# Kernel tuning notes

Measured on AMD Instinct MI355X. Metric: run time of the kernel, lower is better.

Reference implementation:

```python
import jax, jax.numpy as jnp
import numpy as np

N, B, D, K, H = 30000, 16, 32, 8, 8
DIST = 5.0
EPS = 1e-6


def setup_inputs() -> dict:
    key = jax.random.key(0)
    ks = jax.random.split(key, 16)
    sc = 1.0 / np.sqrt(D)
    inp = {
        'pos': jax.random.uniform(ks[0], (N, 3), jnp.float32) * 20.0,
        'node_features': jax.random.normal(ks[1], (N, D), jnp.float32),
        'batch': jnp.sort(jax.random.randint(ks[2], (N,), 0, B, dtype=jnp.int32)),
        'bessel_weights': jnp.linspace(jnp.pi, K * jnp.pi, K).astype(jnp.float32),
        'init_dummy': jax.random.normal(ks[3], (D,), jnp.float32),
        'Wq_dummy': jax.random.normal(ks[4], (D, D), jnp.float32) * sc,
        'Wq_graph': jax.random.normal(ks[5], (D, D), jnp.float32) * sc,
        'Wdot': jax.random.normal(ks[6], (D, D), jnp.float32) * sc,
        'W1_kd': jax.random.normal(ks[7], (K, H), jnp.float32) / np.sqrt(K),
        'W2_kd': jax.random.normal(ks[8], (H, D * D), jnp.float32) / np.sqrt(H),
        'W1_vd': jax.random.normal(ks[9], (K, H), jnp.float32) / np.sqrt(K),
        'W2_vd': jax.random.normal(ks[10], (H, D * D), jnp.float32) / np.sqrt(H),
        'W1_kg': jax.random.normal(ks[11], (K, H), jnp.float32) / np.sqrt(K),
        'W2_kg': jax.random.normal(ks[12], (H, D * D), jnp.float32) / np.sqrt(H),
        'W1_vg': jax.random.normal(ks[13], (K, H), jnp.float32) / np.sqrt(K),
        'W2_vg': jax.random.normal(ks[14], (H, D * D), jnp.float32) / np.sqrt(H),
    }
    return inp


def reference(pos, node_features, batch, bessel_weights, init_dummy,
              Wq_dummy, Wq_graph, Wdot,
              W1_kd, W2_kd, W1_vd, W2_vd, W1_kg, W2_kg, W1_vg, W2_vg):
    scale = 1.0 / np.sqrt(D)

    # --- dummy edge features: per-batch z extents + bessel basis ---
    z = pos[:, 2]                                            # [N]
    z_min = jax.ops.segment_min(z, batch, num_segments=B)    # [B]
    z_max = jax.ops.segment_max(z, batch, num_segments=B)    # [B]
    bot_len = z - z_min[batch] + DIST                        # [N]
    top_len = z_max[batch] + DIST - z                        # [N]

    def bessel(x):  # [N] -> [N,K]
        return jnp.sin(bessel_weights * x[:, None]) / (x[:, None] + EPS)

    edge = jnp.stack([bessel(bot_len), bessel(top_len)], axis=1)  # [N,2,K]

    # --- init dummy node features [B, 2, D] ---
    dummy = jnp.broadcast_to(init_dummy, (B, 2, D))

    def gen_w(W1, W2):  # conditional weight generator (silu MLP)
        return (jax.nn.silu(edge @ W1) @ W2).reshape(N, 2, D, D)

    # --- dummy nodes attend over graph nodes (segment softmax) ---
    wk = gen_w(W1_kd, W2_kd)                                 # [N,2,D,D]
    wv = gen_w(W1_vd, W2_vd)
    q = (dummy @ Wq_dummy)[batch]                            # [N,2,D]
    k = jnp.einsum('nd,nsde->nse', node_features, wk)        # [N,2,D]
    v = jnp.einsum('nd,nsde->nse', node_features, wv)
    s = jnp.einsum('nsq,qk,nsk->ns', q, Wdot, k) * scale     # [N,2]
    m = jax.ops.segment_max(s, batch, num_segments=B)
    e = jnp.exp(s - m[batch])
    zsum = jax.ops.segment_sum(e, batch, num_segments=B)
    attn = e / zsum[batch]                                   # [N,2]
    dummy_new = dummy + jax.ops.segment_sum(attn[..., None] * v, batch, num_segments=B)

    # --- graph nodes attend over (2) dummy nodes ---
    wkg = gen_w(W1_kg, W2_kg)
    wvg = gen_w(W1_vg, W2_vg)
    d_per = dummy_new[batch]                                 # [N,2,D]
    kg = jnp.einsum('nsd,nsde->nse', d_per, wkg)
    vg = jnp.einsum('nsd,nsde->nse', d_per, wvg)
    qg = node_features @ Wq_graph                            # [N,D]
    sg = jnp.einsum('nq,qk,nsk->ns', qg, Wdot, kg) * scale   # [N,2]
    ag = jax.nn.softmax(sg, axis=1)
    x_new = node_features + jnp.einsum('ns,nsd->nd', ag, vg)  # [N,D]
    return x_new
```

## Files before the change

### kernel.cpp

```cpp
#include <hip/hip_runtime.h>
#include <math.h>

#define NN 30000
#define DIST_C 5.0f
#define EPS_C 1e-6f
#define SCALE_C 0.17677669529663687f

#define WS_ZMIN 0
#define WS_ZMAX 16
#define WS_ZSUM 32
#define WS_T    64
#define WS_PK   8256
#define WS_WC   8512
#define WS_AKG  9536
#define WS_AVG  17728

#define NPT 32

__device__ __forceinline__ float silu(float x) { return x / (1.0f + __expf(-x)); }

__device__ __forceinline__ void bessel_edges(float bw0, float x0, float x1, float edge[2][8]) {
    float xs[2]; xs[0] = x0; xs[1] = x1;
#pragma unroll
    for (int s = 0; s < 2; ++s) {
        float x = xs[s];
        float inv = 1.0f / (x + EPS_C);
        float th = bw0 * x;
        float sk, ck;
        __sincosf(th, &sk, &ck);
        float c2 = 2.0f * ck;
        float skm1 = 0.0f;
#pragma unroll
        for (int k = 0; k < 8; ++k) {
            edge[s][k] = sk * inv;
            float nx = c2 * sk - skm1;
            skm1 = sk; sk = nx;
        }
    }
}

__global__ __launch_bounds__(256) void k_pre(const float* __restrict__ pos,
                                             const int* __restrict__ batch,
                                             const float* __restrict__ init_dummy,
                                             const float* __restrict__ Wq_dummy,
                                             const float* __restrict__ Wdot,
                                             const float* __restrict__ W2_kd,
                                             const float* __restrict__ Wq_graph,
                                             float* __restrict__ ws) {
    int t = threadIdx.x, blk = blockIdx.x;
    if (blk < 16) {
        __shared__ int bnd2[2];
        __shared__ float r[8];
        if (t < 2) {
            int target = blk + t;
            int lo = 0, hi = NN;
            while (lo < hi) { int mid = (lo + hi) >> 1; if (batch[mid] < target) lo = mid + 1; else hi = mid; }
            bnd2[t] = lo;
        }
        __syncthreads();
        int s0 = bnd2[0], s1 = bnd2[1];
        float zmn = 3.4e38f, zmx = -3.4e38f;
        for (int i = s0 + t; i < s1; i += 256) {
            float v = pos[3 * i + 2];
            zmn = fminf(zmn, v); zmx = fmaxf(zmx, v);
        }
#pragma unroll
        for (int off = 1; off < 64; off <<= 1) {
            zmn = fminf(zmn, __shfl_xor(zmn, off, 64));
            zmx = fmaxf(zmx, __shfl_xor(zmx, off, 64));
        }
        if ((t & 63) == 0) { r[(t >> 6) * 2] = zmn; r[(t >> 6) * 2 + 1] = zmx; }
        __syncthreads();
        if (t == 0) {
            ws[WS_ZMIN + blk] = fminf(fminf(r[0], r[2]), fminf(r[4], r[6]));
            ws[WS_ZMAX + blk] = fmaxf(fmaxf(r[1], r[3]), fmaxf(r[5], r[7]));
        }
    } else if (blk == 16) {
        __shared__ float qv[32], qW[32];
        if (t < 32) {
            float acc = 0.f;
            for (int d = 0; d < 32; ++d) acc += init_dummy[d] * Wq_dummy[d * 32 + t];
            qv[t] = acc;
        }
        __syncthreads();
        if (t < 32) {
            float acc = 0.f;
            for (int e = 0; e < 32; ++e) acc += qv[e] * Wdot[e * 32 + t];
            qW[t] = acc;
        }
        __syncthreads();
        int h = t >> 5, d = t & 31;
        float acc = 0.f;
        for (int e = 0; e < 32; ++e) acc += W2_kd[h * 1024 + d * 32 + e] * qW[e];
        ws[WS_PK + t] = acc;
    } else if (blk == 17) {
        for (int i = t; i < 1024; i += 256) {
            int d = i >> 5, e = i & 31;
            float acc = 0.f;
            for (int m = 0; m < 32; ++m) acc += Wq_graph[d * 32 + m] * Wdot[m * 32 + e];
            ws[WS_WC + i] = acc;
        }
    } else {
        int idx = blk - 18;
        ws[WS_T + idx * 512 + t] = 0.f;
        ws[WS_T + idx * 512 + 256 + t] = 0.f;
        if (idx == 0 && t < 32) ws[WS_ZSUM + t] = 0.f;
    }
}

__global__ __launch_bounds__(256) void k_phase1(const float* __restrict__ pos,
                                                const int* __restrict__ batch,
                                                const float* __restrict__ nf,
                                                const float* __restrict__ bw,
                                                const float* __restrict__ W1_kd,
                                                const float* __restrict__ W1_vd,
                                                float* __restrict__ ws) {
    __shared__ __align__(16) float Fl[NPT * 36];
    __shared__ float Lw[NPT * 17];
    __shared__ int   Lb[NPT];
    __shared__ __align__(16) float Pk[256];
    __shared__ float W1kd[64], W1vd[64], zsl[32];
    int t = threadIdx.x;
    if (t < 64) { W1kd[t] = W1_kd[t]; W1vd[t] = W1_vd[t]; }
    Pk[t] = ws[WS_PK + t];
    if (t < 32) zsl[t] = 0.f;

    int li = t >> 3, g = t & 7;
    int n0 = blockIdx.x * NPT;
    int n = n0 + li;
    bool valid = n < NN;
    float4 fv4 = make_float4(0.f, 0.f, 0.f, 0.f);
    int b = 0;
    if (valid) {
        b = batch[n];
        fv4 = ((const float4*)nf)[n * 8 + g];
        ((float4*)(Fl + li * 36))[g] = fv4;
        if (g == 0) Lb[li] = b;
    } else {
        if (g == 0) Lb[li] = -1;
    }
    __syncthreads();

    if (valid) {
        float z = pos[3 * n + 2];
        float zminb = ws[WS_ZMIN + b];
        float zmaxb = ws[WS_ZMAX + b];
        float edge[2][8];
        bessel_edges(bw[0], z - zminb + DIST_C, zmaxb + DIST_C - z, edge);

        float up[8];
        const float4* Pk4 = (const float4*)Pk;
#pragma unroll
        for (int h = 0; h < 8; ++h) {
            float4 p = Pk4[h * 8 + g];
            up[h] = fv4.x * p.x + fv4.y * p.y + fv4.z * p.z + fv4.w * p.w;
        }
        float kd0, kd1;
        {
            float p0 = 0.f, p1 = 0.f;
#pragma unroll
            for (int k = 0; k < 8; ++k) {
                float w = W1kd[k * 8 + g];
                p0 += edge[0][k] * w;
                p1 += edge[1][k] * w;
            }
            kd0 = silu(p0); kd1 = silu(p1);
        }
        int lanebase = (t & 63) & 56;
        float sp0 = 0.f, sp1 = 0.f;
#pragma unroll
        for (int h = 0; h < 8; ++h) {
            sp0 += __shfl(kd0, lanebase + h, 64) * up[h];
            sp1 += __shfl(kd1, lanebase + h, 64) * up[h];
        }
#pragma unroll
        for (int m = 1; m < 8; m <<= 1) {
            sp0 += __shfl_xor(sp0, m, 64);
            sp1 += __shfl_xor(sp1, m, 64);
        }
        float ev0 = __expf(sp0 * SCALE_C);
        float ev1 = __expf(sp1 * SCALE_C);
        if (g == 0) {
            atomicAdd(&zsl[b * 2 + 0], ev0);
            atomicAdd(&zsl[b * 2 + 1], ev1);
        }
        float q0 = 0.f, q1 = 0.f;
#pragma unroll
        for (int k = 0; k < 8; ++k) {
            float w = W1vd[k * 8 + g];
            q0 += edge[0][k] * w;
            q1 += edge[1][k] * w;
        }
        Lw[li * 17 + g]     = ev0 * silu(q0);
        Lw[li * 17 + 8 + g] = ev1 * silu(q1);
    }
    __syncthreads();
    if (t < 32 && zsl[t] != 0.f) atomicAdd(&ws[WS_ZSUM + t], zsl[t]);

    int count = NN - n0; if (count > NPT) count = NPT;
    int bf = Lb[0], bl = Lb[count - 1];
    int sh = t & 15, dp = t >> 4;
    for (int b2 = bf; b2 <= bl; ++b2) {
        float a0 = 0.f, a1 = 0.f;
        for (int i = 0; i < count; ++i) {
            if (Lb[i] != b2) continue;
            float w = Lw[i * 17 + sh];
            float2 x = *(const float2*)(Fl + i * 36 + 2 * dp);
            a0 += w * x.x;
            a1 += w * x.y;
        }
        float* Tb = ws + WS_T + b2 * 512 + sh * 32 + 2 * dp;
        atomicAdd(&Tb[0], a0);
        atomicAdd(&Tb[1], a1);
    }
}

__global__ __launch_bounds__(256) void k_batch(const float* __restrict__ init_dummy,
                                               const float* __restrict__ W2_vd,
                                               const float* __restrict__ W2_kg,
                                               const float* __restrict__ W2_vg,
                                               float* __restrict__ ws) {
    int bs = blockIdx.x;
    int b = bs >> 1, s = bs & 1;
    int t = threadIdx.x;
    __shared__ float Tl[256];
    __shared__ float part[256];
    __shared__ float dn[32];
    Tl[t] = ws[WS_T + b * 512 + s * 256 + t];
    __syncthreads();
    {
        int h = t >> 5, e = t & 31;
        float acc = 0.f;
#pragma unroll
        for (int d = 0; d < 32; ++d) acc += Tl[h * 32 + d] * W2_vd[h * 1024 + d * 32 + e];
        part[t] = acc;
    }
    __syncthreads();
    if (t < 32) {
        float acc = 0.f;
#pragma unroll
        for (int h = 0; h < 8; ++h) acc += part[h * 32 + t];
        float zs = ws[WS_ZSUM + b * 2 + s];
        dn[t] = init_dummy[t] + acc / zs;
    }
    __syncthreads();
    {
        int h = t >> 5, e = t & 31;
        float ak = 0.f, av = 0.f;
#pragma unroll
        for (int d = 0; d < 32; ++d) {
            float dv = dn[d];
            ak += dv * W2_kg[h * 1024 + d * 32 + e];
            av += dv * W2_vg[h * 1024 + d * 32 + e];
        }
        ws[WS_AKG + b * 512 + s * 256 + t] = ak;
        ws[WS_AVG + b * 512 + s * 256 + t] = av;
    }
}

__global__ __launch_bounds__(256) void k_fin(const float* __restrict__ pos,
                                             const int* __restrict__ batch,
                                             const float* __restrict__ nf,
                                             const float* __restrict__ bw,
                                             const float* __restrict__ W1_kg,
                                             const float* __restrict__ W1_vg,
                                             const float* __restrict__ ws,
                                             float* __restrict__ out) {
    __shared__ __align__(16) float Wc[1024];
    __shared__ __align__(16) float Fl[NPT * 36];
    __shared__ int   Lb[NPT];
    __shared__ float W1kg[64], W1vg[64];
    __shared__ __align__(16) float AK[2][512], AV[2][512];

    int t = threadIdx.x;
    int li = t >> 3, g = t & 7;
    int lanebase = (t & 63) & 56;
    {
        const float4* Wg4 = (const float4*)(ws + WS_WC);
        ((float4*)Wc)[t] = Wg4[t];
    }
    if (t < 64) { W1kg[t] = W1_kg[t]; W1vg[t] = W1_vg[t]; }

    int n0 = blockIdx.x * NPT;
    int n = n0 + li;
    int count = NN - n0; if (count > NPT) count = NPT;
    bool valid = li < count;
    float4 fv4 = make_float4(0.f, 0.f, 0.f, 0.f);
    float z = 0.f;
    int b = 0;
    if (valid) {
        b = batch[n];
        fv4 = ((const float4*)nf)[n * 8 + g];
        ((float4*)(Fl + li * 36))[g] = fv4;
        z = pos[3 * n + 2];
        if (g == 0) Lb[li] = b;
    }
    __syncthreads();
    int bf = Lb[0], bl = Lb[count - 1];
    int nseg = (bl != bf) ? 2 : 1;

    for (int sl = 0; sl < nseg; ++sl) {
        int bb = sl ? bl : bf;
        const float4* Ag = (const float4*)(ws + WS_AKG + bb * 512);
        const float4* Vg = (const float4*)(ws + WS_AVG + bb * 512);
        if (t < 128) ((float4*)AK[sl])[t] = Ag[t];
        else         ((float4*)AV[sl])[t - 128] = Vg[t - 128];
    }
    __syncthreads();

    if (!valid) return;
    int slot = (b == bf) ? 0 : 1;
    const float4* Ak4 = (const float4*)AK[slot];
    const float4* Av4 = (const float4*)AV[slot];
    const float4* Wc4 = (const float4*)Wc;

    float zminb = ws[WS_ZMIN + b];
    float zmaxb = ws[WS_ZMAX + b];
    float edge[2][8];
    bessel_edges(bw[0], z - zminb + DIST_C, zmaxb + DIST_C - z, edge);

    float sk0, sk1, sv0, sv1;
    {
        float pk0 = 0.f, pk1 = 0.f, pv0 = 0.f, pv1 = 0.f;
#pragma unroll
        for (int k = 0; k < 8; ++k) {
            float wk = W1kg[k * 8 + g];
            float wv = W1vg[k * 8 + g];
            pk0 += edge[0][k] * wk; pk1 += edge[1][k] * wk;
            pv0 += edge[0][k] * wv; pv1 += edge[1][k] * wv;
        }
        sk0 = silu(pk0); sk1 = silu(pk1);
        sv0 = silu(pv0); sv1 = silu(pv1);
    }
    float4 q4 = make_float4(0.f, 0.f, 0.f, 0.f);
    const float* myF = Fl + li * 36;
#pragma unroll
    for (int d = 0; d < 32; ++d) {
        float fd = myF[d];
        float4 w = Wc4[d * 8 + g];
        q4.x += fd * w.x; q4.y += fd * w.y; q4.z += fd * w.z; q4.w += fd * w.w;
    }
    float p0 = 0.f, p1 = 0.f;
#pragma unroll
    for (int h = 0; h < 8; ++h) {
        float4 a0 = Ak4[h * 8 + g];
        float4 a1 = Ak4[64 + h * 8 + g];
        float d0 = q4.x * a0.x + q4.y * a0.y + q4.z * a0.z + q4.w * a0.w;
        float d1 = q4.x * a1.x + q4.y * a1.y + q4.z * a1.z + q4.w * a1.w;
        p0 += __shfl(sk0, lanebase + h, 64) * d0;
        p1 += __shfl(sk1, lanebase + h, 64) * d1;
    }
#pragma unroll
    for (int m = 1; m < 8; m <<= 1) {
        p0 += __shfl_xor(p0, m, 64);
        p1 += __shfl_xor(p1, m, 64);
    }
    float sg0 = p0 * SCALE_C, sg1 = p1 * SCALE_C;
    float mx = fmaxf(sg0, sg1);
    float e0 = __expf(sg0 - mx), e1 = __expf(sg1 - mx);
    float inv = 1.0f / (e0 + e1);
    float ag0 = e0 * inv, ag1 = e1 * inv;

    float4 x4 = fv4;
#pragma unroll
    for (int h = 0; h < 8; ++h) {
        float w0 = ag0 * __shfl(sv0, lanebase + h, 64);
        float w1 = ag1 * __shfl(sv1, lanebase + h, 64);
        float4 a0 = Av4[h * 8 + g];
        float4 a1 = Av4[64 + h * 8 + g];
        x4.x += w0 * a0.x + w1 * a1.x;
        x4.y += w0 * a0.y + w1 * a1.y;
        x4.z += w0 * a0.z + w1 * a1.z;
        x4.w += w0 * a0.w + w1 * a1.w;
    }
    ((float4*)out)[n * 8 + g] = x4;
}

extern "C" void kernel_launch(void* const* d_in, const int* in_sizes, int n_in,
                              void* d_out, int out_size, void* d_ws, size_t ws_size,
                              hipStream_t stream) {
    const float* pos        = (const float*)d_in[0];
    const float* nf         = (const float*)d_in[1];
    const int*   batch      = (const int*)d_in[2];
    const float* bw         = (const float*)d_in[3];
    const float* init_dummy = (const float*)d_in[4];
    const float* Wq_dummy   = (const float*)d_in[5];
    const float* Wq_graph   = (const float*)d_in[6];
    const float* Wdot       = (const float*)d_in[7];
    const float* W1_kd      = (const float*)d_in[8];
    const float* W2_kd      = (const float*)d_in[9];
    const float* W1_vd      = (const float*)d_in[10];
    const float* W2_vd      = (const float*)d_in[11];
    const float* W1_kg      = (const float*)d_in[12];
    const float* W2_kg      = (const float*)d_in[13];
    const float* W1_vg      = (const float*)d_in[14];
    const float* W2_vg      = (const float*)d_in[15];
    float* ws  = (float*)d_ws;
    float* out = (float*)d_out;

    int nblk = (NN + NPT - 1) / NPT;
    hipLaunchKernelGGL(k_pre, dim3(34), dim3(256), 0, stream,
                       pos, batch, init_dummy, Wq_dummy, Wdot, W2_kd, Wq_graph, ws);
    hipLaunchKernelGGL(k_phase1, dim3(nblk), dim3(256), 0, stream,
                       pos, batch, nf, bw, W1_kd, W1_vd, ws);
    hipLaunchKernelGGL(k_batch, dim3(32), dim3(256), 0, stream,
                       init_dummy, W2_vd, W2_kg, W2_vg, ws);
    hipLaunchKernelGGL(k_fin, dim3(nblk), dim3(256), 0, stream,
                       pos, batch, nf, bw, W1_kg, W1_vg, ws, out);
}
```

Baseline: 120.5 us.

## Split dummy-side work across threads: 16 lanes per node, 512-thread blocks

Both per-node kernels now give each node 16 threads instead of 8. Each thread handles one dummy side and one hidden unit, with float2 feature slices, so the two-side Bessel and SiLU work is split across lanes rather than done twice per thread. The phase-1 segmented reduction is rewritten: __syncthreads_count finds the batch boundary and replaces the Lb scan and per-batch loop with at most two linear passes. This aims at more parallelism and less per-thread register and serial work. The cost is a wider shuffle reduction and 512-thread blocks, and the reduction assumes each block spans at most two batch segments.

```diff
diff --git a/kernel.cpp b/kernel.cpp
--- a/kernel.cpp
+++ b/kernel.cpp
@@ -19,23 +19,18 @@
 
 __device__ __forceinline__ float silu(float x) { return x / (1.0f + __expf(-x)); }
 
-__device__ __forceinline__ void bessel_edges(float bw0, float x0, float x1, float edge[2][8]) {
-    float xs[2]; xs[0] = x0; xs[1] = x1;
-#pragma unroll
-    for (int s = 0; s < 2; ++s) {
-        float x = xs[s];
-        float inv = 1.0f / (x + EPS_C);
-        float th = bw0 * x;
-        float sk, ck;
-        __sincosf(th, &sk, &ck);
-        float c2 = 2.0f * ck;
-        float skm1 = 0.0f;
-#pragma unroll
-        for (int k = 0; k < 8; ++k) {
-            edge[s][k] = sk * inv;
-            float nx = c2 * sk - skm1;
-            skm1 = sk; sk = nx;
-        }
+__device__ __forceinline__ void bessel_edge1(float bw0, float x, float edge[8]) {
+    float inv = 1.0f / (x + EPS_C);
+    float th = bw0 * x;
+    float sk, ck;
+    __sincosf(th, &sk, &ck);
+    float c2 = 2.0f * ck;
+    float skm1 = 0.0f;
+#pragma unroll
+    for (int k = 0; k < 8; ++k) {
+        edge[k] = sk * inv;
+        float nx = c2 * sk - skm1;
+        skm1 = sk; sk = nx;
     }
 }
 
@@ -108,7 +103,7 @@
     }
 }
 
-__global__ __launch_bounds__(256) void k_phase1(const float* __restrict__ pos,
+__global__ __launch_bounds__(512) void k_phase1(const float* __restrict__ pos,
                                                 const int* __restrict__ batch,
                                                 const float* __restrict__ nf,
                                                 const float* __restrict__ bw,
@@ -117,101 +112,88 @@
                                                 float* __restrict__ ws) {
     __shared__ __align__(16) float Fl[NPT * 36];
     __shared__ float Lw[NPT * 17];
-    __shared__ int   Lb[NPT];
     __shared__ __align__(16) float Pk[256];
     __shared__ float W1kd[64], W1vd[64], zsl[32];
     int t = threadIdx.x;
     if (t < 64) { W1kd[t] = W1_kd[t]; W1vd[t] = W1_vd[t]; }
-    Pk[t] = ws[WS_PK + t];
+    if (t < 256) Pk[t] = ws[WS_PK + t];
     if (t < 32) zsl[t] = 0.f;
 
-    int li = t >> 3, g = t & 7;
+    int li = t >> 4, g2 = t & 15;
+    int sm = g2 >> 3, hm = g2 & 7;
     int n0 = blockIdx.x * NPT;
     int n = n0 + li;
-    bool valid = n < NN;
-    float4 fv4 = make_float4(0.f, 0.f, 0.f, 0.f);
-    int b = 0;
+    int count = NN - n0; if (count > NPT) count = NPT;
+    bool valid = li < count;
+    int bf = batch[n0], bl = batch[n0 + count - 1];
+    float2 fv2 = make_float2(0.f, 0.f);
+    float z = 0.f;
+    int b = bf;
     if (valid) {
         b = batch[n];
-        fv4 = ((const float4*)nf)[n * 8 + g];
-        ((float4*)(Fl + li * 36))[g] = fv4;
-        if (g == 0) Lb[li] = b;
-    } else {
-        if (g == 0) Lb[li] = -1;
+        fv2 = ((const float2*)nf)[n * 16 + g2];
+        ((float2*)(Fl + li * 36))[g2] = fv2;
+        z = pos[3 * n + 2];
     }
     __syncthreads();
 
     if (valid) {
-        float z = pos[3 * n + 2];
         float zminb = ws[WS_ZMIN + b];
         float zmaxb = ws[WS_ZMAX + b];
-        float edge[2][8];
-        bessel_edges(bw[0], z - zminb + DIST_C, zmaxb + DIST_C - z, edge);
+        float xs = sm ? (zmaxb + DIST_C - z) : (z - zminb + DIST_C);
+        float edge[8];
+        bessel_edge1(bw[0], xs, edge);
 
         float up[8];
-        const float4* Pk4 = (const float4*)Pk;
+        const float2* Pk2 = (const float2*)Pk;
 #pragma unroll
         for (int h = 0; h < 8; ++h) {
-            float4 p = Pk4[h * 8 + g];
-            up[h] = fv4.x * p.x + fv4.y * p.y + fv4.z * p.z + fv4.w * p.w;
-        }
-        float kd0, kd1;
-        {
-            float p0 = 0.f, p1 = 0.f;
-#pragma unroll
-            for (int k = 0; k < 8; ++k) {
-                float w = W1kd[k * 8 + g];
-                p0 += edge[0][k] * w;
-                p1 += edge[1][k] * w;
-            }
-            kd0 = silu(p0); kd1 = silu(p1);
-        }
-        int lanebase = (t & 63) & 56;
+            float2 p = Pk2[h * 16 + g2];
+            up[h] = fv2.x * p.x + fv2.y * p.y;
+        }
+        float pk = 0.f;
+#pragma unroll
+        for (int k = 0; k < 8; ++k) pk += edge[k] * W1kd[k * 8 + hm];
+        float kd = silu(pk);
+
+        int base = (t & 63) & 48;
         float sp0 = 0.f, sp1 = 0.f;
 #pragma unroll
         for (int h = 0; h < 8; ++h) {
-            sp0 += __shfl(kd0, lanebase + h, 64) * up[h];
-            sp1 += __shfl(kd1, lanebase + h, 64) * up[h];
-        }
-#pragma unroll
-        for (int m = 1; m < 8; m <<= 1) {
+            sp0 += __shfl(kd, base + h, 64) * up[h];
+            sp1 += __shfl(kd, base + 8 + h, 64) * up[h];
+        }
+#pragma unroll
+        for (int m = 1; m < 16; m <<= 1) {
             sp0 += __shfl_xor(sp0, m, 64);
             sp1 += __shfl_xor(sp1, m, 64);
         }
         float ev0 = __expf(sp0 * SCALE_C);
         float ev1 = __expf(sp1 * SCALE_C);
-        if (g == 0) {
+        if (g2 == 0) {
             atomicAdd(&zsl[b * 2 + 0], ev0);
             atomicAdd(&zsl[b * 2 + 1], ev1);
         }
-        float q0 = 0.f, q1 = 0.f;
-#pragma unroll
-        for (int k = 0; k < 8; ++k) {
-            float w = W1vd[k * 8 + g];
-            q0 += edge[0][k] * w;
-            q1 += edge[1][k] * w;
-        }
-        Lw[li * 17 + g]     = ev0 * silu(q0);
-        Lw[li * 17 + 8 + g] = ev1 * silu(q1);
-    }
-    __syncthreads();
+        float qv = 0.f;
+#pragma unroll
+        for (int k = 0; k < 8; ++k) qv += edge[k] * W1vd[k * 8 + hm];
+        Lw[li * 17 + g2] = (sm ? ev1 : ev0) * silu(qv);
+    }
+    int nbf = __syncthreads_count(g2 == 0 && valid && b == bf);
     if (t < 32 && zsl[t] != 0.f) atomicAdd(&ws[WS_ZSUM + t], zsl[t]);
 
-    int count = NN - n0; if (count > NPT) count = NPT;
-    int bf = Lb[0], bl = Lb[count - 1];
-    int sh = t & 15, dp = t >> 4;
-    for (int b2 = bf; b2 <= bl; ++b2) {
-        float a0 = 0.f, a1 = 0.f;
-        for (int i = 0; i < count; ++i) {
-            if (Lb[i] != b2) continue;
-            float w = Lw[i * 17 + sh];
-            float2 x = *(const float2*)(Fl + i * 36 + 2 * dp);
-            a0 += w * x.x;
-            a1 += w * x.y;
-        }
-        float* Tb = ws + WS_T + b2 * 512 + sh * 32 + 2 * dp;
-        atomicAdd(&Tb[0], a0);
-        atomicAdd(&Tb[1], a1);
+    int sh = t & 15, dq = t >> 4;
+    {
+        float a = 0.f;
+        for (int i = 0; i < nbf; ++i)
+            a += Lw[i * 17 + sh] * Fl[i * 36 + dq];
+        atomicAdd(ws + WS_T + bf * 512 + sh * 32 + dq, a);
+    }
+    if (nbf < count) {
+        float a = 0.f;
+        for (int i = nbf; i < count; ++i)
+            a += Lw[i * 17 + sh] * Fl[i * 36 + dq];
+        atomicAdd(ws + WS_T + bl * 512 + sh * 32 + dq, a);
     }
 }
 
@@ -258,7 +240,7 @@
     }
 }
 
-__global__ __launch_bounds__(256) void k_fin(const float* __restrict__ pos,
+__global__ __launch_bounds__(512) void k_fin(const float* __restrict__ pos,
                                              const int* __restrict__ batch,
                                              const float* __restrict__ nf,
                                              const float* __restrict__ bw,
@@ -268,90 +250,81 @@
                                              float* __restrict__ out) {
     __shared__ __align__(16) float Wc[1024];
     __shared__ __align__(16) float Fl[NPT * 36];
-    __shared__ int   Lb[NPT];
     __shared__ float W1kg[64], W1vg[64];
     __shared__ __align__(16) float AK[2][512], AV[2][512];
 
     int t = threadIdx.x;
-    int li = t >> 3, g = t & 7;
-    int lanebase = (t & 63) & 56;
-    {
-        const float4* Wg4 = (const float4*)(ws + WS_WC);
-        ((float4*)Wc)[t] = Wg4[t];
-    }
+    int li = t >> 4, g2 = t & 15;
+    int sm = g2 >> 3, hm = g2 & 7;
+    if (t < 256) ((float4*)Wc)[t] = ((const float4*)(ws + WS_WC))[t];
     if (t < 64) { W1kg[t] = W1_kg[t]; W1vg[t] = W1_vg[t]; }
 
     int n0 = blockIdx.x * NPT;
     int n = n0 + li;
     int count = NN - n0; if (count > NPT) count = NPT;
     bool valid = li < count;
-    float4 fv4 = make_float4(0.f, 0.f, 0.f, 0.f);
+    int bf = batch[n0], bl = batch[n0 + count - 1];
+    int nseg = (bl != bf) ? 2 : 1;
+    float2 fv2 = make_float2(0.f, 0.f);
     float z = 0.f;
-    int b = 0;
+    int b = bf;
     if (valid) {
         b = batch[n];
-        fv4 = ((const float4*)nf)[n * 8 + g];
-        ((float4*)(Fl + li * 36))[g] = fv4;
+        fv2 = ((const float2*)nf)[n * 16 + g2];
+        ((float2*)(Fl + li * 36))[g2] = fv2;
         z = pos[3 * n + 2];
-        if (g == 0) Lb[li] = b;
-    }
-    __syncthreads();
-    int bf = Lb[0], bl = Lb[count - 1];
-    int nseg = (bl != bf) ? 2 : 1;
-
+    }
     for (int sl = 0; sl < nseg; ++sl) {
         int bb = sl ? bl : bf;
         const float4* Ag = (const float4*)(ws + WS_AKG + bb * 512);
         const float4* Vg = (const float4*)(ws + WS_AVG + bb * 512);
         if (t < 128) ((float4*)AK[sl])[t] = Ag[t];
-        else         ((float4*)AV[sl])[t - 128] = Vg[t - 128];
+        else if (t < 256) ((float4*)AV[sl])[t - 128] = Vg[t - 128];
     }
     __syncthreads();
 
     if (!valid) return;
     int slot = (b == bf) ? 0 : 1;
-    const float4* Ak4 = (const float4*)AK[slot];
-    const float4* Av4 = (const float4*)AV[slot];
-    const float4* Wc4 = (const float4*)Wc;
+    const float2* Ak2 = (const float2*)AK[slot];
+    const float2* Av2 = (const float2*)AV[slot];
 
     float zminb = ws[WS_ZMIN + b];
     float zmaxb = ws[WS_ZMAX + b];
-    float edge[2][8];
-    bessel_edges(bw[0], z - zminb + DIST_C, zmaxb + DIST_C - z, edge);
-
-    float sk0, sk1, sv0, sv1;
-    {
-        float pk0 = 0.f, pk1 = 0.f, pv0 = 0.f, pv1 = 0.f;
-#pragma unroll
-        for (int k = 0; k < 8; ++k) {
-            float wk = W1kg[k * 8 + g];
-            float wv = W1vg[k * 8 + g];
-            pk0 += edge[0][k] * wk; pk1 += edge[1][k] * wk;
-            pv0 += edge[0][k] * wv; pv1 += edge[1][k] * wv;
-        }
-        sk0 = silu(pk0); sk1 = silu(pk1);
-        sv0 = silu(pv0); sv1 = silu(pv1);
-    }
-    float4 q4 = make_float4(0.f, 0.f, 0.f, 0.f);
+    float xs = sm ? (zmaxb + DIST_C - z) : (z - zminb + DIST_C);
+    float edge[8];
+    bessel_edge1(bw[0], xs, edge);
+
+    float pkk = 0.f, pvv = 0.f;
+#pragma unroll
+    for (int k = 0; k < 8; ++k) {
+        pkk += edge[k] * W1kg[k * 8 + hm];
+        pvv += edge[k] * W1vg[k * 8 + hm];
+    }
+    float skm = silu(pkk);
+    float svm = silu(pvv);
+
+    float2 q2 = make_float2(0.f, 0.f);
     const float* myF = Fl + li * 36;
+    const float2* Wc2 = (const float2*)Wc;
 #pragma unroll
     for (int d = 0; d < 32; ++d) {
         float fd = myF[d];
-        float4 w = Wc4[d * 8 + g];
-        q4.x += fd * w.x; q4.y += fd * w.y; q4.z += fd * w.z; q4.w += fd * w.w;
-    }
+        float2 w = Wc2[d * 16 + g2];
+        q2.x += fd * w.x; q2.y += fd * w.y;
+    }
+    int base = (t & 63) & 48;
     float p0 = 0.f, p1 = 0.f;
 #pragma unroll
     for (int h = 0; h < 8; ++h) {
-        float4 a0 = Ak4[h * 8 + g];
-        float4 a1 = Ak4[64 + h * 8 + g];
-        float d0 = q4.x * a0.x + q4.y * a0.y + q4.z * a0.z + q4.w * a0.w;
-        float d1 = q4.x * a1.x + q4.y * a1.y + q4.z * a1.z + q4.w * a1.w;
-        p0 += __shfl(sk0, lanebase + h, 64) * d0;
-        p1 += __shfl(sk1, lanebase + h, 64) * d1;
-    }
-#pragma unroll
-    for (int m = 1; m < 8; m <<= 1) {
+        float2 a0 = Ak2[h * 16 + g2];
+        float2 a1 = Ak2[128 + h * 16 + g2];
+        float d0 = q2.x * a0.x + q2.y * a0.y;
+        float d1 = q2.x * a1.x + q2.y * a1.y;
+        p0 += __shfl(skm, base + h, 64) * d0;
+        p1 += __shfl(skm, base + 8 + h, 64) * d1;
+    }
+#pragma unroll
+    for (int m = 1; m < 16; m <<= 1) {
         p0 += __shfl_xor(p0, m, 64);
         p1 += __shfl_xor(p1, m, 64);
     }
@@ -361,19 +334,17 @@
     float inv = 1.0f / (e0 + e1);
     float ag0 = e0 * inv, ag1 = e1 * inv;
 
-    float4 x4 = fv4;
+    float2 x2 = fv2;
 #pragma unroll
     for (int h = 0; h < 8; ++h) {
-        float w0 = ag0 * __shfl(sv0, lanebase + h, 64);
-        float w1 = ag1 * __shfl(sv1, lanebase + h, 64);
-        float4 a0 = Av4[h * 8 + g];
-        float4 a1 = Av4[64 + h * 8 + g];
-        x4.x += w0 * a0.x + w1 * a1.x;
-        x4.y += w0 * a0.y + w1 * a1.y;
-        x4.z += w0 * a0.z + w1 * a1.z;
-        x4.w += w0 * a0.w + w1 * a1.w;
-    }
-    ((float4*)out)[n * 8 + g] = x4;
+        float w0 = ag0 * __shfl(svm, base + h, 64);
+        float w1 = ag1 * __shfl(svm, base + 8 + h, 64);
+        float2 a0 = Av2[h * 16 + g2];
+        float2 a1 = Av2[128 + h * 16 + g2];
+        x2.x += w0 * a0.x + w1 * a1.x;
+        x2.y += w0 * a0.y + w1 * a1.y;
+    }
+    ((float2*)out)[n * 16 + g2] = x2;
 }
 
 extern "C" void kernel_launch(void* const* d_in, const int* in_sizes, int n_in,
@@ -401,10 +372,10 @@
     int nblk = (NN + NPT - 1) / NPT;
     hipLaunchKernelGGL(k_pre, dim3(34), dim3(256), 0, stream,
                        pos, batch, init_dummy, Wq_dummy, Wdot, W2_kd, Wq_graph, ws);
-    hipLaunchKernelGGL(k_phase1, dim3(nblk), dim3(256), 0, stream,
+    hipLaunchKernelGGL(k_phase1, dim3(nblk), dim3(512), 0, stream,
                        pos, batch, nf, bw, W1_kd, W1_vd, ws);
     hipLaunchKernelGGL(k_batch, dim3(32), dim3(256), 0, stream,
                        init_dummy, W2_vd, W2_kg, W2_vg, ws);
-    hipLaunchKernelGGL(k_fin, dim3(nblk), dim3(256), 0, stream,
+    hipLaunchKernelGGL(k_fin, dim3(nblk), dim3(512), 0, stream,
                        pos, batch, nf, bw, W1_kg, W1_vg, ws, out);
 }
```

Measured after the change: 122.0 us. About the same (+1.2%).
